# Optimization experiments

Measured on AMD Instinct MI355X. Metric: run time of the kernel, lower is better.

## Reference

```python
import jax, jax.numpy as jnp
import numpy as np

B, S, H, Q = 32, 128, 128, 3  # users, seq_len, hidden_size, quadkey_level
L = Q - 1  # number of mixing scales


def setup_inputs() -> dict:
    key = jax.random.key(0)
    ks = jax.random.split(key, 12)
    trend0 = jax.random.normal(ks[0], (B, S, H), dtype=jnp.float32)
    trend1 = jax.random.normal(ks[1], (B, S, H), dtype=jnp.float32)
    trend2 = jax.random.normal(ks[2], (B, S, H), dtype=jnp.float32)
    # Per-position prefix linears padded into dense tensors, zero-masked beyond
    # the prefix length j+1 so the ragged math is exact:
    #   W1[j, :j+1, :j+1] ~ Linear(j+1, j+1), b1[j, :j+1]
    #   W2[j, :j+1]      ~ Linear(j+1, 1),   b2[j]
    idx = jnp.arange(S)
    pm = (idx[None, :] <= idx[:, None]).astype(jnp.float32)  # [j, s]: s <= j
    W1 = jax.random.normal(ks[3], (L, S, S, S), dtype=jnp.float32) * 0.05
    W1 = W1 * pm[None, :, :, None] * pm[None, :, None, :]
    b1 = jax.random.normal(ks[4], (L, S, S), dtype=jnp.float32) * 0.05 * pm[None]
    W2 = jax.random.normal(ks[5], (L, S, S), dtype=jnp.float32) * 0.05 * pm[None]
    b2 = jax.random.normal(ks[6], (L, S), dtype=jnp.float32) * 0.05
    # shared output MLP: Linear(H,H)->GELU->Linear(H,H); stored as [in, out]
    Wm1 = jax.random.normal(ks[7], (H, H), dtype=jnp.float32) * 0.05
    bm1 = jax.random.normal(ks[8], (H,), dtype=jnp.float32) * 0.05
    Wm2 = jax.random.normal(ks[9], (H, H), dtype=jnp.float32) * 0.05
    bm2 = jax.random.normal(ks[10], (H,), dtype=jnp.float32) * 0.05
    return {"trend0": trend0, "trend1": trend1, "trend2": trend2,
            "W1": W1, "b1": b1, "W2": W2, "b2": b2,
            "Wm1": Wm1, "bm1": bm1, "Wm2": Wm2, "bm2": bm2}


def reference(trend0, trend1, trend2, W1, b1, W2, b2, Wm1, bm1, Wm2, bm2):
    gelu = lambda x: jax.nn.gelu(x, approximate=False)  # torch nn.GELU default
    mlp = lambda x: gelu(x @ Wm1 + bm1) @ Wm2 + bm2

    rev = [trend2, trend1, trend0]  # trend_list reversed
    out_low = rev[0]
    out_high = rev[1]
    outs = [out_low]
    for i in range(Q - 1):
        # vectorized ragged prefix mix: per position j, out_low[:, :j+1] (as [B,H,j+1])
        # -> Linear(j+1,j+1) -> GELU -> Linear(j+1,1). Zero-padding in W1/b1/W2
        # kills all contributions beyond the prefix (GELU(0)=0).
        y1 = jnp.einsum('bsh,jst->bhjt', out_low, W1[i]) + b1[i]  # [B,H,S,S]
        res = jnp.einsum('bhjt,jt->bjh', gelu(y1), W2[i]) + b2[i][None, :, None]
        out_high = out_high + res
        out_low = out_high
        if i + 2 <= Q - 1:
            out_high = rev[i + 2]
        out_low = mlp(out_low)
        outs.append(out_low)
    outs.reverse()
    return tuple(outs)
```

## Files before the change

### kernel.cpp

```cpp
#include <hip/hip_runtime.h>
#include <stdint.h>

#define BSH (32 * 128 * 128)

typedef __attribute__((ext_vector_type(8))) __bf16 bf16x8;
typedef __attribute__((ext_vector_type(4))) float f32x4;

__device__ __forceinline__ unsigned short f2bf(float f) {
  union { float f; unsigned u; } v; v.f = f;
  return (unsigned short)((v.u + 0x7FFFu + ((v.u >> 16) & 1u)) >> 16);
}

__device__ __forceinline__ float fast_exp2(float x) {
#if __has_builtin(__builtin_amdgcn_exp2f)
  return __builtin_amdgcn_exp2f(x);
#else
  float r; asm("v_exp_f32 %0, %1" : "=v"(r) : "v"(x)); return r;
#endif
}
__device__ __forceinline__ float fast_rcp(float x) {
#if __has_builtin(__builtin_amdgcn_rcpf)
  return __builtin_amdgcn_rcpf(x);
#else
  float r; asm("v_rcp_f32 %0, %1" : "=v"(r) : "v"(x)); return r;
#endif
}

__device__ __forceinline__ float gelu_f(float y) {
  float u = y * y;
  float p = __builtin_fmaf(u, 0.044715f, 1.0f) * y;
  float w = fast_exp2(p * 2.30220787f);
  return y - y * fast_rcp(1.0f + w);
}

__device__ __forceinline__ void transpose_block_c(const float* __restrict__ src,
                                                  unsigned short* __restrict__ dst,
                                                  unsigned short* lds) {
  const int tid = threadIdx.x;
  const float4* s4 = (const float4*)(src);
#pragma unroll
  for (int it = 0; it < 16; ++it) {
    int i4 = tid + it * 256;
    float4 v = s4[i4];
    int s = i4 >> 5;
    int t0 = (i4 * 4) & 127;
    unsigned short* pp = lds + s * 136 + t0;
    pp[0] = f2bf(v.x); pp[1] = f2bf(v.y); pp[2] = f2bf(v.z); pp[3] = f2bf(v.w);
  }
  __syncthreads();
#pragma unroll
  for (int it = 0; it < 8; ++it) {
    int c = tid + it * 256;
    int sc = c >> 7, tr = c & 127;
    unsigned short tmp[8] __attribute__((aligned(16)));
#pragma unroll
    for (int e = 0; e < 8; ++e) tmp[e] = lds[(sc * 8 + e) * 136 + tr];
    *(uint4*)(dst + (sc * 128 + tr) * 8) = *(const uint4*)tmp;
  }
}

__global__ __launch_bounds__(256) void prepass_kernel(
    const float* __restrict__ W1, const float* __restrict__ trend2,
    const float* __restrict__ Wm1, const float* __restrict__ Wm2,
    unsigned short* __restrict__ W1Tc, unsigned short* __restrict__ T2c,
    unsigned short* __restrict__ Wm1c, unsigned short* __restrict__ Wm2c,
    float* __restrict__ out2) {
  __shared__ unsigned short lds[128 * 136];
  const int bid = blockIdx.x;
  if (bid < 256) {
    int x = bid & 7, i = bid >> 3;
    int stage = i >> 4, u = i & 15;
    int m = u & 7, half = u >> 3;
    int jpp = x + 8 * m;
    int j = half ? 127 - jpp : jpp;
    int blk = stage * 128 + j;
    transpose_block_c(W1 + blk * 16384, W1Tc + blk * 16384, lds);
  } else if (bid < 288) {
    const int b = bid - 256;
    transpose_block_c(trend2 + b * 16384, T2c + b * 16384, lds);
    const float4* s4 = (const float4*)(trend2 + b * 16384);
    float4* d4 = (float4*)(out2 + b * 16384);
#pragma unroll
    for (int it = 0; it < 16; ++it)
      d4[threadIdx.x + it * 256] = s4[threadIdx.x + it * 256];
  } else if (bid == 288) {
    transpose_block_c(Wm1, Wm1c, lds);
  } else {
    transpose_block_c(Wm2, Wm2c, lds);
  }
}

__global__ __launch_bounds__(256, 3) void mix_kernel(
    const unsigned short* __restrict__ XTc,
    const unsigned short* __restrict__ W1Tj,
    const float* __restrict__ b1j,
    const float* __restrict__ W2j,
    const float* __restrict__ b2j,
    const float* __restrict__ trendR,
    unsigned short* __restrict__ xoutc) {
  __shared__ float res[512];
  const int bid = blockIdx.x;
  const int b = bid >> 6;
  const int jp = bid & 63;
  const int js = jp, jb = 127 - jp;
  const int tid = threadIdx.x;
  const int wave = tid >> 6;
  const int p = wave & 1;
  const int mh = wave >> 1;
  const int lane = tid & 63;
  const int lane15 = lane & 15;
  const int quad = lane >> 4;

  const int nt_s = (js >> 4) + 1, ks_s = (js >> 5) + 1;
  const int nt_b = (jb >> 4) + 1, ks_b = (jb >> 5) + 1;

  const unsigned short* Bp = XTc + b * 16384 + (p * 64 + lane15) * 8;
  const unsigned short* As = W1Tj + js * 16384 + lane15 * 8;
  const unsigned short* Ab = W1Tj + jb * 16384 + lane15 * 8;
  const float C = -2.45546937f;

  bf16x8 Bv[4][4];
#pragma unroll
  for (int ks = 0; ks < 4; ++ks)
    if (ks < ks_b) {
      const int ko = (ks * 4 + quad) * 1024;
      Bv[ks][0] = *(const bf16x8*)(Bp + ko);
      Bv[ks][1] = *(const bf16x8*)(Bp + ko + 128);
      Bv[ks][2] = *(const bf16x8*)(Bp + ko + 256);
      Bv[ks][3] = *(const bf16x8*)(Bp + ko + 384);
    }

  float psum[2][4];
#pragma unroll
  for (int jj = 0; jj < 2; ++jj)
#pragma unroll
    for (int ni = 0; ni < 4; ++ni) psum[jj][ni] = 0.f;

  for (int mt = mh; mt < nt_b; mt += 2) {
    f32x4 acc[4];
#pragma unroll
    for (int ni = 0; ni < 4; ++ni) { f32x4 z = {0.f, 0.f, 0.f, 0.f}; acc[ni] = z; }
    const int mo = mt * 128;
#pragma unroll
    for (int ks = 0; ks < 4; ++ks)
      if (ks < ks_b) {
        bf16x8 a = *(const bf16x8*)(Ab + (ks * 4 + quad) * 1024 + mo);
        acc[0] = __builtin_amdgcn_mfma_f32_16x16x32_bf16(a, Bv[ks][0], acc[0], 0, 0, 0);
        acc[1] = __builtin_amdgcn_mfma_f32_16x16x32_bf16(a, Bv[ks][1], acc[1], 0, 0, 0);
        acc[2] = __builtin_amdgcn_mfma_f32_16x16x32_bf16(a, Bv[ks][2], acc[2], 0, 0, 0);
        acc[3] = __builtin_amdgcn_mfma_f32_16x16x32_bf16(a, Bv[ks][3], acc[3], 0, 0, 0);
      }
    const int tb = mt * 16 + quad * 4;
    float4 b1v = *(const float4*)(b1j + jb * 128 + tb);
    float4 w2v = *(const float4*)(W2j + jb * 128 + tb);
#pragma unroll
    for (int r = 0; r < 4; ++r) {
      float b1r = ((const float*)&b1v)[r];
      float w2r = ((const float*)&w2v)[r];
      float cb = C * b1r;
      float bw = b1r * w2r;
#pragma unroll
      for (int ni = 0; ni < 4; ++ni) {
        float a = acc[ni][r];
        float m = __builtin_fmaf(a, C, cb);
        float e = fast_exp2(m);
        float rr2 = fast_rcp(1.0f + e);
        float yw = __builtin_fmaf(a, w2r, bw);
        psum[1][ni] = __builtin_fmaf(yw, rr2, psum[1][ni]);
      }
    }
  }

  for (int mt = mh; mt < nt_s; mt += 2) {
    f32x4 acc[4];
#pragma unroll
    for (int ni = 0; ni < 4; ++ni) { f32x4 z = {0.f, 0.f, 0.f, 0.f}; acc[ni] = z; }
    const int mo = mt * 128;
#pragma unroll
    for (int ks = 0; ks < 2; ++ks)
      if (ks < ks_s) {
        bf16x8 a = *(const bf16x8*)(As + (ks * 4 + quad) * 1024 + mo);
        acc[0] = __builtin_amdgcn_mfma_f32_16x16x32_bf16(a, Bv[ks][0], acc[0], 0, 0, 0);
        acc[1] = __builtin_amdgcn_mfma_f32_16x16x32_bf16(a, Bv[ks][1], acc[1], 0, 0, 0);
        acc[2] = __builtin_amdgcn_mfma_f32_16x16x32_bf16(a, Bv[ks][2], acc[2], 0, 0, 0);
        acc[3] = __builtin_amdgcn_mfma_f32_16x16x32_bf16(a, Bv[ks][3], acc[3], 0, 0, 0);
      }
    const int tb = mt * 16 + quad * 4;
    float4 b1v = *(const float4*)(b1j + js * 128 + tb);
    float4 w2v = *(const float4*)(W2j + js * 128 + tb);
#pragma unroll
    for (int r = 0; r < 4; ++r) {
      float b1r = ((const float*)&b1v)[r];
      float w2r = ((const float*)&w2v)[r];
      float cb = C * b1r;
      float bw = b1r * w2r;
#pragma unroll
      for (int ni = 0; ni < 4; ++ni) {
        float a = acc[ni][r];
        float m = __builtin_fmaf(a, C, cb);
        float e = fast_exp2(m);
        float rr2 = fast_rcp(1.0f + e);
        float yw = __builtin_fmaf(a, w2r, bw);
        psum[0][ni] = __builtin_fmaf(yw, rr2, psum[0][ni]);
      }
    }
  }

#pragma unroll
  for (int jj = 0; jj < 2; ++jj)
#pragma unroll
    for (int ni = 0; ni < 4; ++ni) {
      float v = psum[jj][ni];
      v += __shfl_xor(v, 16, 64);
      v += __shfl_xor(v, 32, 64);
      psum[jj][ni] = v;
    }

  if (quad == 0) {
#pragma unroll
    for (int jj = 0; jj < 2; ++jj)
#pragma unroll
      for (int ni = 0; ni < 4; ++ni)
        res[wave * 128 + jj * 64 + ni * 16 + lane15] = psum[jj][ni];
  }
  __syncthreads();
  {
    const int l = tid & 15;
    const int ni = (tid >> 4) & 3;
    const int jj = (tid >> 6) & 1;
    const int pp = tid >> 7;
    const int j = jj ? jb : js;
    const int h = pp * 64 + ni * 16 + l;
    float v = res[tid] + res[tid + 256] + b2j[j] +
              trendR[(b * 128 + j) * 128 + h];
    xoutc[b * 16384 + ((h >> 3) * 128 + j) * 8 + (h & 7)] = f2bf(v);
  }
}

__global__ __launch_bounds__(256) void mlp_kernel(
    const unsigned short* __restrict__ Xc,
    const unsigned short* __restrict__ Wm1c,
    const unsigned short* __restrict__ Wm2c,
    const float* __restrict__ bm1,
    const float* __restrict__ bm2,
    float* __restrict__ outf,
    unsigned short* __restrict__ outTc,
    const int write_t) {
  __shared__ __align__(16) unsigned short U[16 * 128];
  __shared__ unsigned short ldsT[16 * 136];
  const int bid = blockIdx.x;
  const int b = bid >> 3;
  const int mb = bid & 7;
  const int tid = threadIdx.x;
  const int wave = tid >> 6;
  const int lane = tid & 63;
  const int lane15 = lane & 15;
  const int quad = lane >> 4;

  const unsigned short* Xb = Xc + b * 16384;

  f32x4 acc[2];
  { f32x4 z = {0.f, 0.f, 0.f, 0.f}; acc[0] = z; acc[1] = z; }
#pragma unroll
  for (int ks = 0; ks < 4; ++ks) {
    int kq = ks * 4 + quad;
    bf16x8 a  = *(const bf16x8*)(Xb + (kq * 128 + mb * 16 + lane15) * 8);
    bf16x8 w0 = *(const bf16x8*)(Wm1c + (kq * 128 + wave * 32 + lane15) * 8);
    bf16x8 w1 = *(const bf16x8*)(Wm1c + (kq * 128 + wave * 32 + 16 + lane15) * 8);
    acc[0] = __builtin_amdgcn_mfma_f32_16x16x32_bf16(a, w0, acc[0], 0, 0, 0);
    acc[1] = __builtin_amdgcn_mfma_f32_16x16x32_bf16(a, w1, acc[1], 0, 0, 0);
  }
#pragma unroll
  for (int ni = 0; ni < 2; ++ni) {
    int n = wave * 32 + ni * 16 + lane15;
    float bv = bm1[n];
#pragma unroll
    for (int r = 0; r < 4; ++r) {
      int jr = quad * 4 + r;
      U[((n >> 3) * 16 + jr) * 8 + (n & 7)] = f2bf(gelu_f(acc[ni][r] + bv));
    }
  }
  __syncthreads();
  { f32x4 z = {0.f, 0.f, 0.f, 0.f}; acc[0] = z; acc[1] = z; }
#pragma unroll
  for (int ks = 0; ks < 4; ++ks) {
    int kq = ks * 4 + quad;
    bf16x8 a  = *(const bf16x8*)(U + (kq * 16 + lane15) * 8);
    bf16x8 w0 = *(const bf16x8*)(Wm2c + (kq * 128 + wave * 32 + lane15) * 8);
    bf16x8 w1 = *(const bf16x8*)(Wm2c + (kq * 128 + wave * 32 + 16 + lane15) * 8);
    acc[0] = __builtin_amdgcn_mfma_f32_16x16x32_bf16(a, w0, acc[0], 0, 0, 0);
    acc[1] = __builtin_amdgcn_mfma_f32_16x16x32_bf16(a, w1, acc[1], 0, 0, 0);
  }
  {
    float* outb = outf + b * 16384 + mb * 16 * 128;
#pragma unroll
    for (int ni = 0; ni < 2; ++ni) {
      int n = wave * 32 + ni * 16 + lane15;
      float bv = bm2[n];
#pragma unroll
      for (int r = 0; r < 4; ++r) {
        int jr = quad * 4 + r;
        float v = acc[ni][r] + bv;
        outb[jr * 128 + n] = v;
        if (write_t) ldsT[jr * 136 + n] = f2bf(v);
      }
    }
  }
  if (write_t) {
    __syncthreads();
    int h = tid & 127, jr8 = tid >> 7;
    unsigned short tmp[8] __attribute__((aligned(16)));
#pragma unroll
    for (int e = 0; e < 8; ++e) tmp[e] = ldsT[(jr8 * 8 + e) * 136 + h];
    *(uint4*)(outTc + b * 16384 + ((mb * 2 + jr8) * 128 + h) * 8) = *(const uint4*)tmp;
  }
}

extern "C" void kernel_launch(void* const* d_in, const int* in_sizes, int n_in,
                              void* d_out, int out_size, void* d_ws, size_t ws_size,
                              hipStream_t stream) {
  (void)in_sizes; (void)n_in; (void)out_size; (void)ws_size;
  const float* trend0 = (const float*)d_in[0];
  const float* trend1 = (const float*)d_in[1];
  const float* trend2 = (const float*)d_in[2];
  const float* W1  = (const float*)d_in[3];
  const float* b1  = (const float*)d_in[4];
  const float* W2  = (const float*)d_in[5];
  const float* b2  = (const float*)d_in[6];
  const float* Wm1 = (const float*)d_in[7];
  const float* bm1 = (const float*)d_in[8];
  const float* Wm2 = (const float*)d_in[9];
  const float* bm2 = (const float*)d_in[10];
  float* out = (float*)d_out;
  char* ws = (char*)d_ws;

  unsigned short* W1Tc = (unsigned short*)(ws);
  unsigned short* T2c  = (unsigned short*)(ws + 8388608);
  unsigned short* x1c  = (unsigned short*)(ws + 9437184);
  unsigned short* A1Tc = (unsigned short*)(ws + 10485760);
  unsigned short* x2c  = (unsigned short*)(ws + 11534336);
  unsigned short* Wm1c = (unsigned short*)(ws + 12582912);
  unsigned short* Wm2c = (unsigned short*)(ws + 12615680);

  prepass_kernel<<<290, 256, 0, stream>>>(W1, trend2, Wm1, Wm2,
                                          W1Tc, T2c, Wm1c, Wm2c, out + 2 * BSH);
  mix_kernel<<<2048, 256, 0, stream>>>(T2c, W1Tc, b1, W2, b2, trend1, x1c);
  mlp_kernel<<<256, 256, 0, stream>>>(x1c, Wm1c, Wm2c, bm1, bm2,
                                      out + BSH, A1Tc, 1);
  mix_kernel<<<2048, 256, 0, stream>>>(A1Tc, W1Tc + 128 * 16384, b1 + 16384,
                                       W2 + 16384, b2 + 128, trend0, x2c);
  mlp_kernel<<<256, 256, 0, stream>>>(x2c, Wm1c, Wm2c, bm1, bm2,
                                      out, (unsigned short*)nullptr, 0);
}
```

Baseline: 137.6 us.

## Fuse output MLP into mix kernel epilogue and drop separate MLP launches

```diff
diff --git a/kernel.cpp b/kernel.cpp
--- a/kernel.cpp
+++ b/kernel.cpp
@@ -90,15 +90,22 @@
   }
 }
 
-__global__ __launch_bounds__(256, 3) void mix_kernel(
+__global__ __launch_bounds__(256, 3) void mix_mlp_kernel(
     const unsigned short* __restrict__ XTc,
     const unsigned short* __restrict__ W1Tj,
     const float* __restrict__ b1j,
     const float* __restrict__ W2j,
     const float* __restrict__ b2j,
     const float* __restrict__ trendR,
-    unsigned short* __restrict__ xoutc) {
+    const unsigned short* __restrict__ Wm1c,
+    const unsigned short* __restrict__ Wm2c,
+    const float* __restrict__ bm1,
+    const float* __restrict__ bm2,
+    float* __restrict__ outA,
+    unsigned short* __restrict__ outTc) {
   __shared__ float res[512];
+  __shared__ __align__(16) float xrow[2][128];
+  __shared__ __align__(16) unsigned short urow[2][128];
   const int bid = blockIdx.x;
   const int b = bid >> 6;
   const int jp = bid & 63;
@@ -226,93 +233,76 @@
   __syncthreads();
   {
     const int l = tid & 15;
-    const int ni = (tid >> 4) & 3;
+    const int nni = (tid >> 4) & 3;
     const int jj = (tid >> 6) & 1;
     const int pp = tid >> 7;
     const int j = jj ? jb : js;
-    const int h = pp * 64 + ni * 16 + l;
+    const int h = pp * 64 + nni * 16 + l;
     float v = res[tid] + res[tid + 256] + b2j[j] +
               trendR[(b * 128 + j) * 128 + h];
-    xoutc[b * 16384 + ((h >> 3) * 128 + j) * 8 + (h & 7)] = f2bf(v);
-  }
-}
-
-__global__ __launch_bounds__(256) void mlp_kernel(
-    const unsigned short* __restrict__ Xc,
-    const unsigned short* __restrict__ Wm1c,
-    const unsigned short* __restrict__ Wm2c,
-    const float* __restrict__ bm1,
-    const float* __restrict__ bm2,
-    float* __restrict__ outf,
-    unsigned short* __restrict__ outTc,
-    const int write_t) {
-  __shared__ __align__(16) unsigned short U[16 * 128];
-  __shared__ unsigned short ldsT[16 * 136];
-  const int bid = blockIdx.x;
-  const int b = bid >> 3;
-  const int mb = bid & 7;
-  const int tid = threadIdx.x;
-  const int wave = tid >> 6;
-  const int lane = tid & 63;
-  const int lane15 = lane & 15;
-  const int quad = lane >> 4;
-
-  const unsigned short* Xb = Xc + b * 16384;
-
-  f32x4 acc[2];
-  { f32x4 z = {0.f, 0.f, 0.f, 0.f}; acc[0] = z; acc[1] = z; }
+    xrow[jj][h] = v;
+  }
+  __syncthreads();
+
+  const int arow = lane15 & 1;
+  bf16x8 af[4];
+#pragma unroll
+  for (int ks = 0; ks < 4; ++ks) {
+    const f32x4* xp = (const f32x4*)&xrow[arow][(ks * 4 + quad) * 8];
+    f32x4 v0 = xp[0], v1 = xp[1];
+    unsigned short t[8] __attribute__((aligned(16)));
+    t[0] = f2bf(v0[0]); t[1] = f2bf(v0[1]); t[2] = f2bf(v0[2]); t[3] = f2bf(v0[3]);
+    t[4] = f2bf(v1[0]); t[5] = f2bf(v1[1]); t[6] = f2bf(v1[2]); t[7] = f2bf(v1[3]);
+    af[ks] = *(const bf16x8*)t;
+  }
+  f32x4 acc1[2];
+  { f32x4 z = {0.f, 0.f, 0.f, 0.f}; acc1[0] = z; acc1[1] = z; }
 #pragma unroll
   for (int ks = 0; ks < 4; ++ks) {
     int kq = ks * 4 + quad;
-    bf16x8 a  = *(const bf16x8*)(Xb + (kq * 128 + mb * 16 + lane15) * 8);
     bf16x8 w0 = *(const bf16x8*)(Wm1c + (kq * 128 + wave * 32 + lane15) * 8);
     bf16x8 w1 = *(const bf16x8*)(Wm1c + (kq * 128 + wave * 32 + 16 + lane15) * 8);
-    acc[0] = __builtin_amdgcn_mfma_f32_16x16x32_bf16(a, w0, acc[0], 0, 0, 0);
-    acc[1] = __builtin_amdgcn_mfma_f32_16x16x32_bf16(a, w1, acc[1], 0, 0, 0);
-  }
-#pragma unroll
-  for (int ni = 0; ni < 2; ++ni) {
-    int n = wave * 32 + ni * 16 + lane15;
-    float bv = bm1[n];
-#pragma unroll
-    for (int r = 0; r < 4; ++r) {
-      int jr = quad * 4 + r;
-      U[((n >> 3) * 16 + jr) * 8 + (n & 7)] = f2bf(gelu_f(acc[ni][r] + bv));
+    acc1[0] = __builtin_amdgcn_mfma_f32_16x16x32_bf16(af[ks], w0, acc1[0], 0, 0, 0);
+    acc1[1] = __builtin_amdgcn_mfma_f32_16x16x32_bf16(af[ks], w1, acc1[1], 0, 0, 0);
+  }
+  if (quad == 0) {
+#pragma unroll
+    for (int ni2 = 0; ni2 < 2; ++ni2) {
+      int n = wave * 32 + ni2 * 16 + lane15;
+      float bv = bm1[n];
+      urow[0][n] = f2bf(gelu_f(acc1[ni2][0] + bv));
+      urow[1][n] = f2bf(gelu_f(acc1[ni2][1] + bv));
     }
   }
   __syncthreads();
-  { f32x4 z = {0.f, 0.f, 0.f, 0.f}; acc[0] = z; acc[1] = z; }
+  bf16x8 uf[4];
+#pragma unroll
+  for (int ks = 0; ks < 4; ++ks)
+    uf[ks] = *(const bf16x8*)&urow[arow][(ks * 4 + quad) * 8];
+  f32x4 acc2[2];
+  { f32x4 z = {0.f, 0.f, 0.f, 0.f}; acc2[0] = z; acc2[1] = z; }
 #pragma unroll
   for (int ks = 0; ks < 4; ++ks) {
     int kq = ks * 4 + quad;
-    bf16x8 a  = *(const bf16x8*)(U + (kq * 16 + lane15) * 8);
     bf16x8 w0 = *(const bf16x8*)(Wm2c + (kq * 128 + wave * 32 + lane15) * 8);
     bf16x8 w1 = *(const bf16x8*)(Wm2c + (kq * 128 + wave * 32 + 16 + lane15) * 8);
-    acc[0] = __builtin_amdgcn_mfma_f32_16x16x32_bf16(a, w0, acc[0], 0, 0, 0);
-    acc[1] = __builtin_amdgcn_mfma_f32_16x16x32_bf16(a, w1, acc[1], 0, 0, 0);
-  }
-  {
-    float* outb = outf + b * 16384 + mb * 16 * 128;
-#pragma unroll
-    for (int ni = 0; ni < 2; ++ni) {
-      int n = wave * 32 + ni * 16 + lane15;
+    acc2[0] = __builtin_amdgcn_mfma_f32_16x16x32_bf16(uf[ks], w0, acc2[0], 0, 0, 0);
+    acc2[1] = __builtin_amdgcn_mfma_f32_16x16x32_bf16(uf[ks], w1, acc2[1], 0, 0, 0);
+  }
+  if (quad == 0) {
+#pragma unroll
+    for (int ni2 = 0; ni2 < 2; ++ni2) {
+      int n = wave * 32 + ni2 * 16 + lane15;
       float bv = bm2[n];
 #pragma unroll
-      for (int r = 0; r < 4; ++r) {
-        int jr = quad * 4 + r;
-        float v = acc[ni][r] + bv;
-        outb[jr * 128 + n] = v;
-        if (write_t) ldsT[jr * 136 + n] = f2bf(v);
-      }
-    }
-  }
-  if (write_t) {
-    __syncthreads();
-    int h = tid & 127, jr8 = tid >> 7;
-    unsigned short tmp[8] __attribute__((aligned(16)));
-#pragma unroll
-    for (int e = 0; e < 8; ++e) tmp[e] = ldsT[(jr8 * 8 + e) * 136 + h];
-    *(uint4*)(outTc + b * 16384 + ((mb * 2 + jr8) * 128 + h) * 8) = *(const uint4*)tmp;
+      for (int r = 0; r < 2; ++r) {
+        int j = r ? jb : js;
+        float v = acc2[ni2][r] + bv;
+        outA[(b * 128 + j) * 128 + n] = v;
+        if (outTc)
+          outTc[b * 16384 + ((j >> 3) * 128 + n) * 8 + (j & 7)] = f2bf(v);
+      }
+    }
   }
 }
 
@@ -336,19 +326,17 @@
 
   unsigned short* W1Tc = (unsigned short*)(ws);
   unsigned short* T2c  = (unsigned short*)(ws + 8388608);
-  unsigned short* x1c  = (unsigned short*)(ws + 9437184);
-  unsigned short* A1Tc = (unsigned short*)(ws + 10485760);
-  unsigned short* x2c  = (unsigned short*)(ws + 11534336);
-  unsigned short* Wm1c = (unsigned short*)(ws + 12582912);
-  unsigned short* Wm2c = (unsigned short*)(ws + 12615680);
+  unsigned short* A1Tc = (unsigned short*)(ws + 9437184);
+  unsigned short* Wm1c = (unsigned short*)(ws + 10485760);
+  unsigned short* Wm2c = (unsigned short*)(ws + 10518528);
 
   prepass_kernel<<<290, 256, 0, stream>>>(W1, trend2, Wm1, Wm2,
                                           W1Tc, T2c, Wm1c, Wm2c, out + 2 * BSH);
-  mix_kernel<<<2048, 256, 0, stream>>>(T2c, W1Tc, b1, W2, b2, trend1, x1c);
-  mlp_kernel<<<256, 256, 0, stream>>>(x1c, Wm1c, Wm2c, bm1, bm2,
-                                      out + BSH, A1Tc, 1);
-  mix_kernel<<<2048, 256, 0, stream>>>(A1Tc, W1Tc + 128 * 16384, b1 + 16384,
-                                       W2 + 16384, b2 + 128, trend0, x2c);
-  mlp_kernel<<<256, 256, 0, stream>>>(x2c, Wm1c, Wm2c, bm1, bm2,
-                                      out, (unsigned short*)nullptr, 0);
-}
+  mix_mlp_kernel<<<2048, 256, 0, stream>>>(T2c, W1Tc, b1, W2, b2, trend1,
+                                           Wm1c, Wm2c, bm1, bm2,
+                                           out + BSH, A1Tc);
+  mix_mlp_kernel<<<2048, 256, 0, stream>>>(A1Tc, W1Tc + 128 * 16384, b1 + 16384,
+                                           W2 + 16384, b2 + 128, trend0,
+                                           Wm1c, Wm2c, bm1, bm2,
+                                           out, (unsigned short*)nullptr);
+}
```

After: 140.6 us. +2.2%, slower.
